# Optimization experiments

Measured on AMD Instinct MI355X. Metric: run time of the kernel, lower is better.

Reference implementation:

```python
import jax, jax.numpy as jnp
import numpy as np

B, S, D, H = 8, 1024, 768, 12
DK = D // H  # 64


def setup_inputs() -> dict:
    key = jax.random.key(0)
    ks = jax.random.split(key, 11)
    scale = 1.0 / np.sqrt(D)
    inp = {
        "query": jax.random.normal(ks[0], (B, S, D), jnp.float32),
        "key": jax.random.normal(ks[1], (B, S, D), jnp.float32),
        "value": jax.random.normal(ks[2], (B, S, D), jnp.float32),
        "Wq": jax.random.normal(ks[3], (D, D), jnp.float32) * scale,
        "bq": jnp.zeros((D,), jnp.float32),
        "Wk": jax.random.normal(ks[4], (D, D), jnp.float32) * scale,
        "bk": jnp.zeros((D,), jnp.float32),
        "Wv": jax.random.normal(ks[5], (D, D), jnp.float32) * scale,
        "bv": jnp.zeros((D,), jnp.float32),
        "Wd": jax.random.normal(ks[6], (D, D), jnp.float32) * scale,
        "bd": jnp.zeros((D,), jnp.float32),
    }
    return inp


def reference(query, key, value, Wq, bq, Wk, bk, Wv, bv, Wd, bd):
    # QKV projections (torch Linear equivalent: x @ W + b with W stored [in,out])
    q = query @ Wq + bq  # [B,S,D]
    k = key @ Wk + bk
    v = value @ Wv + bv
    # split heads -> [B,H,S,DK]
    q = q.reshape(B, S, H, DK).transpose(0, 2, 1, 3)
    k = k.reshape(B, S, H, DK).transpose(0, 2, 1, 3)
    v = v.reshape(B, S, H, DK).transpose(0, 2, 1, 3)
    scores = jnp.einsum("bhqd,bhkd->bhqk", q, k) / jnp.sqrt(jnp.float32(DK))
    weights = jax.nn.softmax(scores, axis=-1)  # attn dropout = identity (eval)
    ctx = jnp.einsum("bhqk,bhkd->bhqd", weights, v)
    context = ctx.transpose(0, 2, 1, 3).reshape(B, S, D)
    hidden_states = context @ Wd + bd  # out dropout = identity (eval)
    return (hidden_states, context)
```

## Files before the change

### kernel.cpp

```cpp
#include <hip/hip_runtime.h>
#include <hip/hip_bf16.h>
#include <math.h>

constexpr int Bc = 8;
constexpr int Sc = 1024;
constexpr int Dc = 768;
constexpr int Hc = 12;
constexpr int DKc = 64;
constexpr int BSc = Bc * Sc;
constexpr size_t HEAD_ELEMS = (size_t)Bc * Hc * Sc * DKc;
constexpr size_t OUT_ELEMS  = (size_t)Bc * Sc * Dc;

typedef __attribute__((ext_vector_type(8))) short short8;
typedef __attribute__((ext_vector_type(4))) short short4v;
typedef __attribute__((ext_vector_type(4))) float f32x4;

__device__ __forceinline__ short f2bf(float x) {
  __hip_bfloat16 h = __float2bfloat16(x);
  short r;
  __builtin_memcpy(&r, &h, 2);
  return r;
}

__device__ __forceinline__ void gload16(const void* g, void* l) {
  __builtin_amdgcn_global_load_lds(
      (const __attribute__((address_space(1))) void*)g,
      (__attribute__((address_space(3))) void*)l, 16, 0, 0);
}

__global__ __launch_bounds__(256) void cast3(
    const float* __restrict__ q, const float* __restrict__ k,
    const float* __restrict__ v, __hip_bfloat16* __restrict__ dq,
    __hip_bfloat16* __restrict__ dk, __hip_bfloat16* __restrict__ dv) {
  const int which = blockIdx.y;
  const float* src = (which == 0) ? q : (which == 1) ? k : v;
  __hip_bfloat16* dst = (which == 0) ? dq : (which == 1) ? dk : dv;
  const size_t i = ((size_t)blockIdx.x * 256 + threadIdx.x) * 8;
  const float4 f0 = *reinterpret_cast<const float4*>(src + i);
  const float4 f1 = *reinterpret_cast<const float4*>(src + i + 4);
  short8 s;
  s[0] = f2bf(f0.x); s[1] = f2bf(f0.y); s[2] = f2bf(f0.z); s[3] = f2bf(f0.w);
  s[4] = f2bf(f1.x); s[5] = f2bf(f1.y); s[6] = f2bf(f1.z); s[7] = f2bf(f1.w);
  *reinterpret_cast<short8*>(dst + i) = s;
}

__global__ __launch_bounds__(256) void wtrans4(
    const float* __restrict__ W0, const float* __restrict__ W1,
    const float* __restrict__ W2, const float* __restrict__ W3,
    __hip_bfloat16* __restrict__ Wt0) {
  __shared__ float t[32][33];
  const int z = blockIdx.z;
  const float* W = (z == 0) ? W0 : (z == 1) ? W1 : (z == 2) ? W2 : W3;
  __hip_bfloat16* Wt = Wt0 + (size_t)z * Dc * Dc;
  const int tx = threadIdx.x & 31, ty = threadIdx.x >> 5;
  const int bx = blockIdx.x * 32;
  const int by = blockIdx.y * 32;
  #pragma unroll
  for (int i = 0; i < 32; i += 8)
    t[ty + i][tx] = W[(size_t)(by + ty + i) * Dc + bx + tx];
  __syncthreads();
  #pragma unroll
  for (int i = 0; i < 32; i += 8)
    Wt[(size_t)(bx + ty + i) * Dc + by + tx] = __float2bfloat16(t[tx][ty + i]);
}

__device__ __forceinline__ void stage_tiles(
    const __hip_bfloat16* A, const __hip_bfloat16* Wt, int row0, int col0,
    int k0, int wv, int lane, __hip_bfloat16* bufA, __hip_bfloat16* bufB) {
  #pragma unroll
  for (int j = 0; j < 2; j++) {
    const int rr = j * 64 + wv * 16;
    const int r = rr + (lane >> 2);
    const int kc = k0 + (lane & 3) * 8;
    gload16(A + (size_t)(row0 + r) * Dc + kc, bufA + rr * 32);
    gload16(Wt + (size_t)(col0 + r) * Dc + kc, bufB + rr * 32);
  }
}

__device__ __forceinline__ void compute_tiles(
    const __hip_bfloat16* bufA, const __hip_bfloat16* bufB, int wr, int wc,
    int l15, int g, f32x4 (&acc)[4][4]) {
  short8 a[4], b[4];
  #pragma unroll
  for (int ai = 0; ai < 4; ai++)
    a[ai] = *reinterpret_cast<const short8*>(
        &bufA[(wr * 64 + ai * 16 + l15) * 32 + g * 8]);
  #pragma unroll
  for (int bj = 0; bj < 4; bj++)
    b[bj] = *reinterpret_cast<const short8*>(
        &bufB[(wc * 64 + bj * 16 + l15) * 32 + g * 8]);
  #pragma unroll
  for (int ai = 0; ai < 4; ai++)
    #pragma unroll
    for (int bj = 0; bj < 4; bj++)
      acc[ai][bj] = __builtin_amdgcn_mfma_f32_16x16x32_bf16(
          a[ai], b[bj], acc[ai][bj], 0, 0, 0);
}

#define GEMM_PIPELINE(A_, Wt_)                                          \
  stage_tiles(A_, Wt_, row0, col0, 0, wv, lane, As0, Bs0);              \
  __syncthreads();                                                      \
  for (int t = 0; t < 24; t += 2) {                                     \
    stage_tiles(A_, Wt_, row0, col0, (t + 1) * 32, wv, lane, As1, Bs1); \
    compute_tiles(As0, Bs0, wr, wc, l15, g, acc);                       \
    __syncthreads();                                                    \
    if (t + 2 < 24)                                                     \
      stage_tiles(A_, Wt_, row0, col0, (t + 2) * 32, wv, lane, As0, Bs0);\
    compute_tiles(As1, Bs1, wr, wc, l15, g, acc);                       \
    __syncthreads();                                                    \
  }

__global__ __launch_bounds__(256) void gemm_qkv(
    const __hip_bfloat16* __restrict__ Aq, const __hip_bfloat16* __restrict__ Ak,
    const __hip_bfloat16* __restrict__ Av, const __hip_bfloat16* __restrict__ Wt0,
    const float* __restrict__ bq, const float* __restrict__ bk,
    const float* __restrict__ bv, __hip_bfloat16* __restrict__ out0) {
  __shared__ __hip_bfloat16 As0[128 * 32], Bs0[128 * 32];
  __shared__ __hip_bfloat16 As1[128 * 32], Bs1[128 * 32];

  const int tid = threadIdx.x;
  const int lane = tid & 63;
  const int wv = tid >> 6;
  const int l15 = lane & 15;
  const int g = lane >> 4;
  const int wr = wv >> 1, wc = wv & 1;

  const int proj = blockIdx.y;
  const __hip_bfloat16* A = (proj == 0) ? Aq : (proj == 1) ? Ak : Av;
  const float* bias = (proj == 0) ? bq : (proj == 1) ? bk : bv;
  const __hip_bfloat16* Wt = Wt0 + (size_t)proj * Dc * Dc;
  __hip_bfloat16* out = out0 + (size_t)proj * HEAD_ELEMS;

  const int orig = blockIdx.x;
  const int swz = (orig & 7) * 48 + (orig >> 3);
  const int row0 = (swz / (Dc / 128)) * 128;
  const int col0 = (swz % (Dc / 128)) * 128;

  f32x4 acc[4][4];
  #pragma unroll
  for (int ai = 0; ai < 4; ai++)
    #pragma unroll
    for (int bj = 0; bj < 4; bj++) acc[ai][bj] = f32x4{0.f, 0.f, 0.f, 0.f};

  GEMM_PIPELINE(A, Wt)

  const int mb = row0 + wr * 64, nb = col0 + wc * 64;
  if (proj < 2) {
    #pragma unroll
    for (int ai = 0; ai < 4; ai++)
      #pragma unroll
      for (int bj = 0; bj < 4; bj++) {
        const int n = nb + bj * 16 + l15;
        const int h_ = n >> 6, dk = n & 63;
        const float bn = bias[n];
        #pragma unroll
        for (int reg = 0; reg < 4; reg++) {
          const int m = mb + ai * 16 + g * 4 + reg;
          const int b_ = m >> 10, s_ = m & 1023;
          out[(((size_t)(b_ * Hc + h_)) * Sc + s_) * DKc + dk] =
              __float2bfloat16(acc[ai][bj][reg] + bn);
        }
      }
  } else {
    #pragma unroll
    for (int ai = 0; ai < 4; ai++)
      #pragma unroll
      for (int bj = 0; bj < 4; bj++) {
        const int n = nb + bj * 16 + l15;
        const int h_ = n >> 6, dk = n & 63;
        const float bn = bias[n];
        const int m0 = mb + ai * 16 + g * 4;
        const int b_ = m0 >> 10, s0 = m0 & 1023;
        short4v sv;
        sv[0] = f2bf(acc[ai][bj][0] + bn);
        sv[1] = f2bf(acc[ai][bj][1] + bn);
        sv[2] = f2bf(acc[ai][bj][2] + bn);
        sv[3] = f2bf(acc[ai][bj][3] + bn);
        *reinterpret_cast<short4v*>(
            &out[(((size_t)(b_ * Hc + h_)) * DKc + dk) * Sc + s0]) = sv;
      }
  }
}

__global__ __launch_bounds__(256) void gemm_o(
    const __hip_bfloat16* __restrict__ A, const __hip_bfloat16* __restrict__ Wt,
    const float* __restrict__ bias, float* __restrict__ out) {
  __shared__ __hip_bfloat16 As0[128 * 32], Bs0[128 * 32];
  __shared__ __hip_bfloat16 As1[128 * 32], Bs1[128 * 32];

  const int tid = threadIdx.x;
  const int lane = tid & 63;
  const int wv = tid >> 6;
  const int l15 = lane & 15;
  const int g = lane >> 4;
  const int wr = wv >> 1, wc = wv & 1;

  const int orig = blockIdx.x;
  const int swz = (orig & 7) * 48 + (orig >> 3);
  const int row0 = (swz / (Dc / 128)) * 128;
  const int col0 = (swz % (Dc / 128)) * 128;

  f32x4 acc[4][4];
  #pragma unroll
  for (int ai = 0; ai < 4; ai++)
    #pragma unroll
    for (int bj = 0; bj < 4; bj++) acc[ai][bj] = f32x4{0.f, 0.f, 0.f, 0.f};

  GEMM_PIPELINE(A, Wt)

  const int mb = row0 + wr * 64, nb = col0 + wc * 64;
  #pragma unroll
  for (int ai = 0; ai < 4; ai++)
    #pragma unroll
    for (int bj = 0; bj < 4; bj++) {
      const int n = nb + bj * 16 + l15;
      const float bn = bias[n];
      #pragma unroll
      for (int reg = 0; reg < 4; reg++) {
        const int m = mb + ai * 16 + g * 4 + reg;
        out[(size_t)m * Dc + n] = acc[ai][bj][reg] + bn;
      }
    }
}

__global__ __launch_bounds__(256) void attn_mfma(
    const __hip_bfloat16* __restrict__ Q, const __hip_bfloat16* __restrict__ K,
    const __hip_bfloat16* __restrict__ Vt, float* __restrict__ ctx,
    __hip_bfloat16* __restrict__ ctxb) {
  __shared__ __hip_bfloat16 Ks[64 * 64];
  __shared__ __hip_bfloat16 Vs[64 * 64];

  const int tid = threadIdx.x;
  const int lane = tid & 63;
  const int w = tid >> 6;
  const int l15 = lane & 15;
  const int g = lane >> 4;

  const int cpx = gridDim.x >> 3;
  const int bid = blockIdx.x;
  const int wid = (bid & 7) * cpx + (bid >> 3);
  const int bh = wid >> 4;
  const int qt = wid & 15;
  const int qbase = qt * 64 + w * 16;

  const __hip_bfloat16* Qb = Q + (size_t)bh * Sc * DKc;
  const __hip_bfloat16* Kb = K + (size_t)bh * Sc * DKc;
  const __hip_bfloat16* Vtb = Vt + (size_t)bh * DKc * Sc;

  short8 qf[2];
  {
    const __hip_bfloat16* qp = Qb + (size_t)(qbase + l15) * DKc + g * 8;
    qf[0] = *reinterpret_cast<const short8*>(qp);
    qf[1] = *reinterpret_cast<const short8*>(qp + 32);
  }

  f32x4 Oacc[4];
  #pragma unroll
  for (int dt = 0; dt < 4; dt++) Oacc[dt] = f32x4{0.f, 0.f, 0.f, 0.f};
  float m_run = -1e30f, l_run = 0.f;

  constexpr float SM_SCALE = 0.125f * 1.44269504088896340736f;

  for (int kt = 0; kt < Sc; kt += 64) {
    __syncthreads();
    #pragma unroll
    for (int it = 0; it < 2; it++) {
      const int tt = tid + it * 256;
      const int row = tt >> 3, s = tt & 7;
      const float4 kv = *reinterpret_cast<const float4*>(
          Kb + (size_t)(kt + row) * DKc + s * 8);
      const float4 vv = *reinterpret_cast<const float4*>(
          Vtb + (size_t)row * Sc + kt + s * 8);
      const int off = row * 128 + ((s ^ (row & 7)) << 4);
      *reinterpret_cast<float4*>((char*)Ks + off) = kv;
      *reinterpret_cast<float4*>((char*)Vs + off) = vv;
    }
    __syncthreads();

    f32x4 sacc[4];
    #pragma unroll
    for (int mt = 0; mt < 4; mt++) sacc[mt] = f32x4{0.f, 0.f, 0.f, 0.f};
    #pragma unroll
    for (int c = 0; c < 2; c++) {
      #pragma unroll
      for (int mt = 0; mt < 4; mt++) {
        const int row = mt * 16 + l15;
        const short8 kf = *reinterpret_cast<const short8*>(
            (char*)Ks + row * 128 + (((g + 4 * c) ^ (row & 7)) << 4));
        sacc[mt] =
            __builtin_amdgcn_mfma_f32_16x16x32_bf16(kf, qf[c], sacc[mt], 0, 0, 0);
      }
    }

    float tmax = -1e30f;
    #pragma unroll
    for (int s = 0; s < 4; s++)
      #pragma unroll
      for (int r = 0; r < 4; r++) tmax = fmaxf(tmax, sacc[s][r]);
    tmax = fmaxf(tmax, __shfl_xor(tmax, 16));
    tmax = fmaxf(tmax, __shfl_xor(tmax, 32));
    const float mnew = fmaxf(m_run, tmax);
    const float alpha = __builtin_amdgcn_exp2f((m_run - mnew) * SM_SCALE);
    m_run = mnew;
    float wgt[4][4];
    float wsum = 0.f;
    #pragma unroll
    for (int s = 0; s < 4; s++)
      #pragma unroll
      for (int r = 0; r < 4; r++) {
        wgt[s][r] = __builtin_amdgcn_exp2f((sacc[s][r] - mnew) * SM_SCALE);
        wsum += wgt[s][r];
      }
    l_run = l_run * alpha + wsum;

    float ar[4];
    #pragma unroll
    for (int r = 0; r < 4; r++) ar[r] = __shfl(alpha, g * 4 + r);
    #pragma unroll
    for (int dt = 0; dt < 4; dt++)
      #pragma unroll
      for (int r = 0; r < 4; r++) Oacc[dt][r] *= ar[r];

    short8 pa[2];
    #pragma unroll
    for (int c = 0; c < 2; c++)
      #pragma unroll
      for (int i = 0; i < 8; i++) pa[c][i] = f2bf(wgt[2 * c + (i >> 2)][i & 3]);

    #pragma unroll
    for (int dt = 0; dt < 4; dt++) {
      const int row = dt * 16 + l15;
      const int rb2 = row * 128;
      const int sw = row & 7;
      const int gl = (g & 1) * 8;
      const int gh = g >> 1;
      #pragma unroll
      for (int c = 0; c < 2; c++) {
        const short4v v0 = *reinterpret_cast<const short4v*>(
            (char*)Vs + rb2 + ((((4 * c + 0) + gh) ^ sw) << 4) + gl);
        const short4v v1 = *reinterpret_cast<const short4v*>(
            (char*)Vs + rb2 + ((((4 * c + 2) + gh) ^ sw) << 4) + gl);
        const short8 vf =
            __builtin_shufflevector(v0, v1, 0, 1, 2, 3, 4, 5, 6, 7);
        Oacc[dt] =
            __builtin_amdgcn_mfma_f32_16x16x32_bf16(pa[c], vf, Oacc[dt], 0, 0, 0);
      }
    }
  }

  l_run += __shfl_xor(l_run, 16);
  l_run += __shfl_xor(l_run, 32);
  float linv[4];
  #pragma unroll
  for (int r = 0; r < 4; r++) linv[r] = 1.0f / __shfl(l_run, g * 4 + r);

  const int b_ = bh / Hc, h_ = bh % Hc;
  #pragma unroll
  for (int dt = 0; dt < 4; dt++)
    #pragma unroll
    for (int r = 0; r < 4; r++) {
      const int qa = qbase + g * 4 + r;
      const size_t idx =
          ((size_t)(b_ * Sc + qa)) * Dc + h_ * 64 + dt * 16 + l15;
      const float val = Oacc[dt][r] * linv[r];
      ctx[idx] = val;
      ctxb[idx] = __float2bfloat16(val);
    }
}

extern "C" void kernel_launch(void* const* d_in, const int* in_sizes, int n_in,
                              void* d_out, int out_size, void* d_ws,
                              size_t ws_size, hipStream_t stream) {
  const float* query = (const float*)d_in[0];
  const float* key_  = (const float*)d_in[1];
  const float* value = (const float*)d_in[2];
  const float* Wq = (const float*)d_in[3];
  const float* bq = (const float*)d_in[4];
  const float* Wk = (const float*)d_in[5];
  const float* bk = (const float*)d_in[6];
  const float* Wv = (const float*)d_in[7];
  const float* bv = (const float*)d_in[8];
  const float* Wd = (const float*)d_in[9];
  const float* bd = (const float*)d_in[10];

  float* out = (float*)d_out;
  float* hidden = out;
  float* context = out + OUT_ELEMS;

  __hip_bfloat16* Aq = (__hip_bfloat16*)hidden;
  __hip_bfloat16* Ak = Aq + OUT_ELEMS;

  __hip_bfloat16* Qw  = (__hip_bfloat16*)d_ws;
  __hip_bfloat16* Kw  = Qw + HEAD_ELEMS;
  __hip_bfloat16* Vtw = Kw + HEAD_ELEMS;
  __hip_bfloat16* WtQ = Vtw + HEAD_ELEMS;
  __hip_bfloat16* WtD = WtQ + 3 * (size_t)Dc * Dc;
  __hip_bfloat16* Av  = WtQ + 4 * (size_t)Dc * Dc;
  __hip_bfloat16* ctxb = Av;

  wtrans4<<<dim3(Dc / 32, Dc / 32, 4), 256, 0, stream>>>(Wq, Wk, Wv, Wd, WtQ);
  cast3<<<dim3(OUT_ELEMS / 8 / 256, 3), 256, 0, stream>>>(
      query, key_, value, Aq, Ak, Av);

  gemm_qkv<<<dim3((BSc / 128) * (Dc / 128), 3), 256, 0, stream>>>(
      Aq, Ak, Av, WtQ, bq, bk, bv, Qw);

  attn_mfma<<<Bc * Hc * (Sc / 64), 256, 0, stream>>>(Qw, Kw, Vtw, context,
                                                     ctxb);

  gemm_o<<<(BSc / 128) * (Dc / 128), 256, 0, stream>>>(ctxb, WtD, bd, hidden);
}
```

Before: 271.0 us.

## Double-buffer K/V tiles in attention and use 64-row tiles for output GEMM

The attention kernel now prefetches the next K/V tile into registers while computing on the current shared-memory buffer, then writes it to a second LDS buffer. This overlaps global load latency with MFMA work and removes one barrier per tile. The output projection GEMM switches to 64x128 tiles with its own double-buffered pipeline, doubling block count to improve CU occupancy and tail balance. The cost is twice the LDS in attention, extra registers for the prefetch, and less reuse per block in the GEMM.

```diff
diff --git a/kernel.cpp b/kernel.cpp
--- a/kernel.cpp
+++ b/kernel.cpp
@@ -182,11 +182,11 @@
   }
 }
 
-__global__ __launch_bounds__(256) void gemm_o(
+__global__ __launch_bounds__(256) void gemm_o64(
     const __hip_bfloat16* __restrict__ A, const __hip_bfloat16* __restrict__ Wt,
     const float* __restrict__ bias, float* __restrict__ out) {
-  __shared__ __hip_bfloat16 As0[128 * 32], Bs0[128 * 32];
-  __shared__ __hip_bfloat16 As1[128 * 32], Bs1[128 * 32];
+  __shared__ __hip_bfloat16 As0[64 * 32], As1[64 * 32];
+  __shared__ __hip_bfloat16 Bs0[128 * 32], Bs1[128 * 32];
 
   const int tid = threadIdx.x;
   const int lane = tid & 63;
@@ -196,21 +196,59 @@
   const int wr = wv >> 1, wc = wv & 1;
 
   const int orig = blockIdx.x;
-  const int swz = (orig & 7) * 48 + (orig >> 3);
-  const int row0 = (swz / (Dc / 128)) * 128;
+  const int swz = (orig & 7) * 96 + (orig >> 3);
+  const int row0 = (swz / (Dc / 128)) * 64;
   const int col0 = (swz % (Dc / 128)) * 128;
 
-  f32x4 acc[4][4];
-  #pragma unroll
-  for (int ai = 0; ai < 4; ai++)
+  f32x4 acc[2][4];
+  #pragma unroll
+  for (int ai = 0; ai < 2; ai++)
     #pragma unroll
     for (int bj = 0; bj < 4; bj++) acc[ai][bj] = f32x4{0.f, 0.f, 0.f, 0.f};
 
-  GEMM_PIPELINE(A, Wt)
-
-  const int mb = row0 + wr * 64, nb = col0 + wc * 64;
-  #pragma unroll
-  for (int ai = 0; ai < 4; ai++)
+  auto STAGE = [&](int k0, __hip_bfloat16* bufA, __hip_bfloat16* bufB) {
+    const int r = wv * 16 + (lane >> 2);
+    const int kc = k0 + (lane & 3) * 8;
+    gload16(A + (size_t)(row0 + r) * Dc + kc, bufA + (wv * 16) * 32);
+    #pragma unroll
+    for (int j = 0; j < 2; j++) {
+      const int rr = j * 64 + wv * 16;
+      const int rn = rr + (lane >> 2);
+      gload16(Wt + (size_t)(col0 + rn) * Dc + kc, bufB + rr * 32);
+    }
+  };
+  auto COMP = [&](const __hip_bfloat16* bufA, const __hip_bfloat16* bufB) {
+    short8 a[2], b[4];
+    #pragma unroll
+    for (int ai = 0; ai < 2; ai++)
+      a[ai] = *reinterpret_cast<const short8*>(
+          &bufA[(wr * 32 + ai * 16 + l15) * 32 + g * 8]);
+    #pragma unroll
+    for (int bj = 0; bj < 4; bj++)
+      b[bj] = *reinterpret_cast<const short8*>(
+          &bufB[(wc * 64 + bj * 16 + l15) * 32 + g * 8]);
+    #pragma unroll
+    for (int ai = 0; ai < 2; ai++)
+      #pragma unroll
+      for (int bj = 0; bj < 4; bj++)
+        acc[ai][bj] = __builtin_amdgcn_mfma_f32_16x16x32_bf16(
+            a[ai], b[bj], acc[ai][bj], 0, 0, 0);
+  };
+
+  STAGE(0, As0, Bs0);
+  __syncthreads();
+  for (int t = 0; t < 24; t += 2) {
+    STAGE((t + 1) * 32, As1, Bs1);
+    COMP(As0, Bs0);
+    __syncthreads();
+    if (t + 2 < 24) STAGE((t + 2) * 32, As0, Bs0);
+    COMP(As1, Bs1);
+    __syncthreads();
+  }
+
+  const int mb = row0 + wr * 32, nb = col0 + wc * 64;
+  #pragma unroll
+  for (int ai = 0; ai < 2; ai++)
     #pragma unroll
     for (int bj = 0; bj < 4; bj++) {
       const int n = nb + bj * 16 + l15;
@@ -227,8 +265,8 @@
     const __hip_bfloat16* __restrict__ Q, const __hip_bfloat16* __restrict__ K,
     const __hip_bfloat16* __restrict__ Vt, float* __restrict__ ctx,
     __hip_bfloat16* __restrict__ ctxb) {
-  __shared__ __hip_bfloat16 Ks[64 * 64];
-  __shared__ __hip_bfloat16 Vs[64 * 64];
+  __shared__ __hip_bfloat16 Ks0[64 * 64], Vs0[64 * 64];
+  __shared__ __hip_bfloat16 Ks1[64 * 64], Vs1[64 * 64];
 
   const int tid = threadIdx.x;
   const int lane = tid & 63;
@@ -261,22 +299,29 @@
 
   constexpr float SM_SCALE = 0.125f * 1.44269504088896340736f;
 
-  for (int kt = 0; kt < Sc; kt += 64) {
-    __syncthreads();
+  float4 kr[2], vr[2];
+  auto LOADT = [&](int kt) {
     #pragma unroll
     for (int it = 0; it < 2; it++) {
       const int tt = tid + it * 256;
       const int row = tt >> 3, s = tt & 7;
-      const float4 kv = *reinterpret_cast<const float4*>(
+      kr[it] = *reinterpret_cast<const float4*>(
           Kb + (size_t)(kt + row) * DKc + s * 8);
-      const float4 vv = *reinterpret_cast<const float4*>(
+      vr[it] = *reinterpret_cast<const float4*>(
           Vtb + (size_t)row * Sc + kt + s * 8);
+    }
+  };
+  auto WRITET = [&](__hip_bfloat16* Kd, __hip_bfloat16* Vd) {
+    #pragma unroll
+    for (int it = 0; it < 2; it++) {
+      const int tt = tid + it * 256;
+      const int row = tt >> 3, s = tt & 7;
       const int off = row * 128 + ((s ^ (row & 7)) << 4);
-      *reinterpret_cast<float4*>((char*)Ks + off) = kv;
-      *reinterpret_cast<float4*>((char*)Vs + off) = vv;
-    }
-    __syncthreads();
-
+      *reinterpret_cast<float4*>((char*)Kd + off) = kr[it];
+      *reinterpret_cast<float4*>((char*)Vd + off) = vr[it];
+    }
+  };
+  auto COMPUTE = [&](const __hip_bfloat16* Ksb, const __hip_bfloat16* Vsb) {
     f32x4 sacc[4];
     #pragma unroll
     for (int mt = 0; mt < 4; mt++) sacc[mt] = f32x4{0.f, 0.f, 0.f, 0.f};
@@ -286,7 +331,7 @@
       for (int mt = 0; mt < 4; mt++) {
         const int row = mt * 16 + l15;
         const short8 kf = *reinterpret_cast<const short8*>(
-            (char*)Ks + row * 128 + (((g + 4 * c) ^ (row & 7)) << 4));
+            (const char*)Ksb + row * 128 + (((g + 4 * c) ^ (row & 7)) << 4));
         sacc[mt] =
             __builtin_amdgcn_mfma_f32_16x16x32_bf16(kf, qf[c], sacc[mt], 0, 0, 0);
       }
@@ -337,14 +382,32 @@
       #pragma unroll
       for (int c = 0; c < 2; c++) {
         const short4v v0 = *reinterpret_cast<const short4v*>(
-            (char*)Vs + rb2 + ((((4 * c + 0) + gh) ^ sw) << 4) + gl);
+            (const char*)Vsb + rb2 + ((((4 * c + 0) + gh) ^ sw) << 4) + gl);
         const short4v v1 = *reinterpret_cast<const short4v*>(
-            (char*)Vs + rb2 + ((((4 * c + 2) + gh) ^ sw) << 4) + gl);
+            (const char*)Vsb + rb2 + ((((4 * c + 2) + gh) ^ sw) << 4) + gl);
         const short8 vf =
             __builtin_shufflevector(v0, v1, 0, 1, 2, 3, 4, 5, 6, 7);
         Oacc[dt] =
             __builtin_amdgcn_mfma_f32_16x16x32_bf16(pa[c], vf, Oacc[dt], 0, 0, 0);
       }
+    }
+  };
+
+  LOADT(0);
+  WRITET(Ks0, Vs0);
+  __syncthreads();
+
+  #pragma unroll 1
+  for (int j = 0; j < 8; j++) {
+    LOADT(j * 128 + 64);
+    COMPUTE(Ks0, Vs0);
+    WRITET(Ks1, Vs1);
+    __syncthreads();
+    if (j < 7) LOADT(j * 128 + 128);
+    COMPUTE(Ks1, Vs1);
+    if (j < 7) {
+      WRITET(Ks0, Vs0);
+      __syncthreads();
     }
   }
 
@@ -408,5 +471,5 @@
   attn_mfma<<<Bc * Hc * (Sc / 64), 256, 0, stream>>>(Qw, Kw, Vtw, context,
                                                      ctxb);
 
-  gemm_o<<<(BSc / 128) * (Dc / 128), 256, 0, stream>>>(ctxb, WtD, bd, hidden);
-}
+  gemm_o64<<<(BSc / 64) * (Dc / 128), 256, 0, stream>>>(ctxb, WtD, bd, hidden);
+}
```

Measured after the change: 310.9 us. 14.7% more time.
